# Kernel optimization log

Hardware: AMD Instinct MI355X
Metric: run time of the kernel (lower is better)

## Reference

```python
import jax, jax.numpy as jnp
import numpy as np

H = 64
N_NODES = 12000
N_EDGES = 50000


def setup_inputs() -> dict:
    key = jax.random.key(0)
    ks = jax.random.split(key, 16)
    s = 1.0 / np.sqrt(H)
    inp = {
        "node": jax.random.normal(ks[0], (N_NODES, H), jnp.float32),
        "edge": jax.random.normal(ks[1], (N_EDGES, H), jnp.float32),
        "hidden_feats": jax.random.normal(ks[2], (N_NODES, H), jnp.float32),
        "src": jax.random.randint(ks[3], (N_EDGES,), 0, N_NODES, jnp.int32),
        "dst": jax.random.randint(ks[4], (N_EDGES,), 0, N_NODES, jnp.int32),
        # edge_network: Linear(H, 2H) -> ReLU -> Linear(2H, H*H)
        "W1": jax.random.uniform(ks[5], (2 * H, H), jnp.float32, -s, s),
        "b1": jax.random.uniform(ks[6], (2 * H,), jnp.float32, -s, s),
        "W2": jax.random.uniform(ks[7], (H * H, 2 * H), jnp.float32, -1 / np.sqrt(2 * H), 1 / np.sqrt(2 * H)),
        "b2": jax.random.uniform(ks[8], (H * H,), jnp.float32, -1 / np.sqrt(2 * H), 1 / np.sqrt(2 * H)),
        # GRUCell params (torch layout: [3H, H], gate order r,z,n)
        "W_ih": jax.random.uniform(ks[9], (3 * H, H), jnp.float32, -s, s),
        "W_hh": jax.random.uniform(ks[10], (3 * H, H), jnp.float32, -s, s),
        "b_ih": jax.random.uniform(ks[11], (3 * H,), jnp.float32, -s, s),
        "b_hh": jax.random.uniform(ks[12], (3 * H,), jnp.float32, -s, s),
        # LayerNorm params
        "gamma": jnp.ones((H,), jnp.float32),
        "beta": jnp.zeros((H,), jnp.float32),
    }
    return inp


def _gru_cell(x, h, W_ih, W_hh, b_ih, b_hh):
    gi = x @ W_ih.T + b_ih  # [N, 3H]
    gh = h @ W_hh.T + b_hh  # [N, 3H]
    r = jax.nn.sigmoid(gi[:, :H] + gh[:, :H])
    z = jax.nn.sigmoid(gi[:, H:2 * H] + gh[:, H:2 * H])
    n = jnp.tanh(gi[:, 2 * H:] + r * gh[:, 2 * H:])
    return (1.0 - z) * n + z * h


def reference(node, edge, hidden_feats, src, dst, W1, b1, W2, b2,
              W_ih, W_hh, b_ih, b_hh, gamma, beta):
    n_nodes = node.shape[0]
    # edge network -> per-edge [H,H] weight matrices
    eh = jax.nn.relu(edge @ W1.T + b1)                      # [E, 2H]
    Wedge = (eh @ W2.T + b2).reshape(-1, H, H)              # [E, H, H]
    # gather src feats, per-edge matmul (row-vector @ matrix), scatter-sum to dst
    msg = jnp.einsum('eh,ehk->ek', node[src], Wedge)        # [E, H]
    agg = jax.ops.segment_sum(msg, dst, num_segments=n_nodes)  # [N, H]
    new_node_feats = jax.nn.relu(agg)
    out = _gru_cell(new_node_feats, hidden_feats, W_ih, W_hh, b_ih, b_hh)
    # LayerNorm (eps=1e-5)
    mu = jnp.mean(out, axis=-1, keepdims=True)
    var = jnp.var(out, axis=-1, keepdims=True)
    out = (out - mu) * jax.lax.rsqrt(var + 1e-5) * gamma + beta
    return out
```

## Files before the change

### kernel.cpp

```cpp
#include <hip/hip_runtime.h>

#define H 64
#define NEDGE 50000
#define NNODE 12000
#define EPAD 50176

typedef _Float16 f16;
typedef _Float16 h8 __attribute__((ext_vector_type(8)));
typedef float f4 __attribute__((ext_vector_type(4)));
typedef float fv16 __attribute__((ext_vector_type(16)));

#define O_EDGEH 0ull
#define O_W2G   6422528ull
#define O_B2G   7471104ull
#define O_W1G   7479296ull
#define O_WG    7495680ull
#define O_AGG   7561216ull

__device__ __forceinline__ fv16 zero16() {
  fv16 z;
#pragma unroll
  for (int i = 0; i < 16; ++i) z[i] = 0.f;
  return z;
}

__global__ __launch_bounds__(256) void k_prep(const float* __restrict__ edge, const float* __restrict__ W1,
                                              const float* __restrict__ W2, const float* __restrict__ b2,
                                              const float* __restrict__ Wih, const float* __restrict__ Whh,
                                              f16* __restrict__ edgeh, f16* __restrict__ w1g, f16* __restrict__ w2g,
                                              f16* __restrict__ b2g, f16* __restrict__ wg, float* __restrict__ agg) {
  int bid = blockIdx.x;
  int t = threadIdx.x;
  if (bid < 750) {
    int id = bid * 256 + t;
    *(f4*)(agg + (long)id * 4) = (f4){0.f, 0.f, 0.f, 0.f};
    return;
  }
  if (bid < 2318) {
    long id8 = (long)(bid - 750) * 256 + t;
    long e = id8 >> 3;
    int c = (int)(id8 & 7) * 8;
    h8 o = {};
    if (e < NEDGE) {
      const float* p = edge + e * 64 + c;
      f4 v0 = *(const f4*)p, v1 = *(const f4*)(p + 4);
#pragma unroll
      for (int j = 0; j < 4; ++j) { o[j] = (f16)v0[j]; o[4 + j] = (f16)v1[j]; }
    }
    *(h8*)(edgeh + e * 64 + c) = o;
    return;
  }
  if (bid < 4366) {
    int id = (bid - 2318) * 256 + t;
    int i = id & 7, l = (id >> 3) & 63, nh = (id >> 9) & 1, s = (id >> 10) & 7, h = id >> 13;
    int n = nh * 32 + (l & 31), j = s * 16 + ((l >> 5) << 3) + i;
    w2g[id] = (f16)W2[(h * 64 + n) * 128 + j];
    return;
  }
  if (bid < 4382) {
    int id = (bid - 4366) * 256 + t;
    int i = id & 7, l = (id >> 3) & 63, nh = (id >> 9) & 1, s = id >> 10;
    int n = nh * 32 + (l & 31), k = s * 16 + ((l >> 5) << 3) + i;
    b2g[id] = (f16)b2[k * 64 + n];
    return;
  }
  if (bid < 4414) {
    int id = (bid - 4382) * 256 + t;
    int i = id & 7, l = (id >> 3) & 63, nt = (id >> 9) & 3, s = id >> 11;
    int n = nt * 32 + (l & 31), k = s * 16 + ((l >> 5) << 3) + i;
    w1g[id] = (f16)W1[n * 64 + k];
    return;
  }
  {
    int id = (bid - 4414) * 256 + t;
    int ii = id & 7, l = (id >> 3) & 63, tt = (id >> 9) & 15, s = id >> 13;
    int k = s * 32 + ((l >> 4) << 3) + ii, n = tt * 16 + (l & 15);
    float v;
    if (n < 128) v = (k < 64) ? Wih[n * 64 + k] : Whh[n * 64 + (k - 64)];
    else if (n < 192) v = (k < 64) ? Wih[n * 64 + k] : 0.f;
    else v = (k < 64) ? 0.f : Whh[(n - 64) * 64 + (k - 64)];
    wg[id] = (f16)v;
  }
}

__global__ __launch_bounds__(256, 3) void k_msg(const float* __restrict__ node,
                                                const int* __restrict__ src, const int* __restrict__ dst,
                                                const f16* __restrict__ edgeh, const f16* __restrict__ w1g,
                                                const f16* __restrict__ w2g, const float* __restrict__ b1,
                                                float* __restrict__ agg) {
  __shared__ __align__(16) char lds[26368];
  f16* eh_s = (f16*)lds;
  f16* vT = (f16*)(lds + 16384);
  int* sdst = (int*)(lds + 25600);
  float* b1s = (float*)(lds + 25856);

  int t = threadIdx.x;
  int bid = blockIdx.x;
  int e_base = (bid >> 1) * 64;
  int hs = bid & 1;

  if (t < 64) {
    int eg = e_base + t;
    sdst[t] = (eg < NEDGE) ? dst[eg] : 0;
  } else if (t < 192) {
    b1s[t - 64] = b1[t - 64];
  }
  {
    int m = t >> 2, q = t & 3;
    int eg = e_base + m;
    int si = (eg < NEDGE) ? src[eg] : 0;
    const f4* nr = (const f4*)(node + (long)si * 64 + q * 16);
    f4 v0 = nr[0], v1 = nr[1], v2 = nr[2], v3 = nr[3];
    h8 p0, p1;
#pragma unroll
    for (int j = 0; j < 4; ++j) {
      p0[j] = (f16)v0[j]; p0[4 + j] = (f16)v1[j];
      p1[j] = (f16)v2[j]; p1[4 + j] = (f16)v3[j];
    }
    *(h8*)(vT + m * 72 + q * 16) = p0;
    *(h8*)(vT + m * 72 + q * 16 + 8) = p1;
  }
  __syncthreads();

  int wave = t >> 6, lane = t & 63;
  int l31 = lane & 31, lh = lane >> 5;
  int kh = wave & 1, wn = wave >> 1;

  {
    h8 afr[2][4];
#pragma unroll
    for (int mt = 0; mt < 2; ++mt)
#pragma unroll
      for (int s = 0; s < 4; ++s)
        afr[mt][s] = *(const h8*)(edgeh + (long)(e_base + mt * 32 + l31) * 64 + s * 16 + lh * 8);
    h8 bfr[4];
#pragma unroll
    for (int s = 0; s < 4; ++s)
      bfr[s] = *(const h8*)(w1g + ((s * 4 + wave) * 64 + lane) * 8);
    fv16 acc_eh[2];
    acc_eh[0] = zero16(); acc_eh[1] = zero16();
#pragma unroll
    for (int s = 0; s < 4; ++s)
#pragma unroll
      for (int mt = 0; mt < 2; ++mt)
        acc_eh[mt] = __builtin_amdgcn_mfma_f32_32x32x16_f16(afr[mt][s], bfr[s], acc_eh[mt], 0, 0, 0);
#pragma unroll
    for (int mt = 0; mt < 2; ++mt)
#pragma unroll
      for (int r = 0; r < 16; ++r) {
        int row = (r & 3) + 8 * (r >> 2) + 4 * lh;
        int e = mt * 32 + row;
        int n = wave * 32 + l31;
        float val = fmaxf(acc_eh[mt][r] + b1s[n], 0.f);
        int o = n >> 3;
        eh_s[e * 128 + ((o ^ (e & 15)) << 3) + (n & 7)] = (f16)val;
      }
  }
  __syncthreads();

  h8 ehreg[2][4];
#pragma unroll
  for (int mt = 0; mt < 2; ++mt) {
    int e = mt * 32 + l31;
#pragma unroll
    for (int s = 0; s < 4; ++s) {
      int o = ((kh * 4 + s) * 2 + lh) ^ (e & 15);
      ehreg[mt][s] = *(const h8*)(eh_s + e * 128 + o * 8);
    }
  }
  __syncthreads();

  fv16 acc[2];
  acc[0] = zero16(); acc[1] = zero16();
  const f16* vrow = vT + l31 * 72;

  const f16* bb = w2g + kh * 4096 + wn * 512 + (long)lane * 8;
  int hfirst = hs << 5;
  int hlast = hfirst + 31;

  h8 bA[4], bB[4];
#pragma unroll
  for (int s = 0; s < 4; ++s) bA[s] = *(const h8*)(bb + (long)hfirst * 8192 + s * 1024);

  auto step = [&](h8 (&bc)[4], h8 (&bn)[4], int h, f16 v0, f16 v1) {
    if (h < hlast) {
      const f16* bp = bb + (long)(h + 1) * 8192;
#pragma unroll
      for (int s = 0; s < 4; ++s) bn[s] = *(const h8*)(bp + s * 1024);
    }
#pragma unroll
    for (int s = 0; s < 4; ++s) {
      h8 bf = bc[s];
      h8 a0 = ehreg[0][s] * v0;
      acc[0] = __builtin_amdgcn_mfma_f32_32x32x16_f16(a0, bf, acc[0], 0, 0, 0);
      h8 a1 = ehreg[1][s] * v1;
      acc[1] = __builtin_amdgcn_mfma_f32_32x32x16_f16(a1, bf, acc[1], 0, 0, 0);
    }
  };

#pragma unroll 1
  for (int hb = hs * 4; hb < hs * 4 + 4; ++hb) {
    h8 vh0 = *(const h8*)(vrow + hb * 8);
    h8 vh1 = *(const h8*)(vrow + 32 * 72 + hb * 8);
#pragma unroll
    for (int hh = 0; hh < 8; ++hh) {
      int h = hb * 8 + hh;
      if (hh & 1) step(bB, bA, h, vh0[hh], vh1[hh]);
      else step(bA, bB, h, vh0[hh], vh1[hh]);
    }
  }

  if (hs) {
    const f16* bt = w2g + (long)64 * 8192 + kh * 2048 + wn * 512 + (long)lane * 8;
#pragma unroll
    for (int sw = 0; sw < 2; ++sw) {
      h8 bf = *(const h8*)(bt + sw * 1024);
#pragma unroll
      for (int mt = 0; mt < 2; ++mt) {
        h8 a = *(const h8*)(vrow + mt * 32 * 72 + ((kh * 2 + sw) * 2 + lh) * 8);
        acc[mt] = __builtin_amdgcn_mfma_f32_32x32x16_f16(a, bf, acc[mt], 0, 0, 0);
      }
    }
  }

  {
    float* red = (float*)lds;
    float* mybase = red + wave * 1024;
    auto wr = [&](const fv16& a) {
#pragma unroll
      for (int r = 0; r < 4; ++r) {
        f4 q = {a[4 * r], a[4 * r + 1], a[4 * r + 2], a[4 * r + 3]};
        *(f4*)(mybase + r * 256 + lane * 4) = q;
      }
    };
    if (!kh) wr(acc[1]); else wr(acc[0]);
    __syncthreads();
    const float* pb = red + (wave ^ 1) * 1024;
    auto rd = [&](fv16& a) {
#pragma unroll
      for (int r = 0; r < 4; ++r) {
        f4 q = *(const f4*)(pb + r * 256 + lane * 4);
        a[4 * r] += q[0]; a[4 * r + 1] += q[1]; a[4 * r + 2] += q[2]; a[4 * r + 3] += q[3];
      }
    };
    if (!kh) rd(acc[0]); else rd(acc[1]);
  }

  {
    int n = wn * 32 + l31;
    const fv16& a = kh ? acc[1] : acc[0];
#pragma unroll
    for (int r = 0; r < 16; ++r) {
      int el = kh * 32 + (r & 3) + 8 * (r >> 2) + 4 * lh;
      if (e_base + el < NEDGE) atomicAdd(&agg[(long)sdst[el] * 64 + n], a[r]);
    }
  }
}

__global__ __launch_bounds__(256) void k_node(const float* __restrict__ agg, const float* __restrict__ hid,
                                              const f16* __restrict__ wg,
                                              const float* __restrict__ bih, const float* __restrict__ bhh,
                                              const float* __restrict__ gamma, const float* __restrict__ beta,
                                              float* __restrict__ out) {
  __shared__ __align__(16) f16 xh_s[128 * 136];
  __shared__ float bsum[128], bin_s[64], bhn_s[64], gam_s[64], bet_s[64];
  int t = threadIdx.x;
  int n0 = blockIdx.x * 128;

  if (t < 128) bsum[t] = bih[t] + bhh[t];
  else if (t < 192) bin_s[t - 128] = bih[t];
  else bhn_s[t - 192] = bhh[t - 64];
  if (t < 64) gam_s[t] = gamma[t];
  else if (t < 128) bet_s[t - 64] = beta[t - 64];

  {
    int m = t >> 1, half = t & 1;
    int mg = n0 + m;
    bool vld = mg < NNODE;
    const float* sp = half ? (hid + (long)mg * 64) : (agg + (long)mg * 64);
#pragma unroll
    for (int jj = 0; jj < 8; ++jj) {
      f4 v0 = {0, 0, 0, 0}, v1 = {0, 0, 0, 0};
      if (vld) { v0 = *(const f4*)(sp + jj * 8); v1 = *(const f4*)(sp + jj * 8 + 4); }
      h8 pk;
#pragma unroll
      for (int m2 = 0; m2 < 4; ++m2) {
        pk[m2] = (f16)(half ? v0[m2] : fmaxf(v0[m2], 0.f));
        pk[4 + m2] = (f16)(half ? v1[m2] : fmaxf(v1[m2], 0.f));
      }
      *(h8*)(xh_s + m * 136 + half * 64 + jj * 8) = pk;
    }
  }
  __syncthreads();

  int wave = t >> 6, lane = t & 63;
  int l15 = lane & 15, lq = lane >> 4;

  f4 acc[2][16];
#pragma unroll
  for (int g = 0; g < 2; ++g)
#pragma unroll
    for (int tt = 0; tt < 16; ++tt) acc[g][tt] = (f4){0.f, 0.f, 0.f, 0.f};

#pragma unroll
  for (int s = 0; s < 4; ++s) {
    h8 a0 = *(const h8*)(xh_s + (wave * 32 + l15) * 136 + s * 32 + lq * 8);
    h8 a1 = *(const h8*)(xh_s + (wave * 32 + 16 + l15) * 136 + s * 32 + lq * 8);
#pragma unroll
    for (int tt = 0; tt < 16; ++tt) {
      h8 b = *(const h8*)(wg + ((s * 16 + tt) * 64 + lane) * 8);
      acc[0][tt] = __builtin_amdgcn_mfma_f32_16x16x32_f16(a0, b, acc[0][tt], 0, 0, 0);
      acc[1][tt] = __builtin_amdgcn_mfma_f32_16x16x32_f16(a1, b, acc[1][tt], 0, 0, 0);
    }
  }

#pragma unroll
  for (int g = 0; g < 2; ++g)
#pragma unroll
    for (int r = 0; r < 4; ++r) {
      int mg = n0 + wave * 32 + g * 16 + lq * 4 + r;
      bool vld = mg < NNODE;
      float o[4], ssum = 0.f, s2 = 0.f;
#pragma unroll
      for (int t0 = 0; t0 < 4; ++t0) {
        int f = t0 * 16 + l15;
        float rpre = acc[g][t0][r] + bsum[f];
        float zpre = acc[g][4 + t0][r] + bsum[64 + f];
        float ginv = acc[g][8 + t0][r] + bin_s[f];
        float ghnv = acc[g][12 + t0][r] + bhn_s[f];
        float rr = 1.f / (1.f + __expf(-rpre));
        float zz = 1.f / (1.f + __expf(-zpre));
        float hv = vld ? hid[(long)mg * 64 + f] : 0.f;
        float nn = tanhf(ginv + rr * ghnv);
        float oo = (1.f - zz) * nn + zz * hv;
        o[t0] = oo; ssum += oo; s2 += oo * oo;
      }
#pragma unroll
      for (int d = 1; d < 16; d <<= 1) {
        ssum += __shfl_xor(ssum, d);
        s2 += __shfl_xor(s2, d);
      }
      float mu = ssum * (1.f / 64.f);
      float var = s2 * (1.f / 64.f) - mu * mu;
      float rstd = rsqrtf(var + 1e-5f);
      if (vld)
#pragma unroll
        for (int t0 = 0; t0 < 4; ++t0) {
          int f = t0 * 16 + l15;
          out[(long)mg * 64 + f] = (o[t0] - mu) * rstd * gam_s[f] + bet_s[f];
        }
    }
}

extern "C" void kernel_launch(void* const* d_in, const int* in_sizes, int n_in,
                              void* d_out, int out_size, void* d_ws, size_t ws_size,
                              hipStream_t stream) {
  const float* node = (const float*)d_in[0];
  const float* edge = (const float*)d_in[1];
  const float* hid = (const float*)d_in[2];
  const int* src = (const int*)d_in[3];
  const int* dst = (const int*)d_in[4];
  const float* W1 = (const float*)d_in[5];
  const float* b1 = (const float*)d_in[6];
  const float* W2 = (const float*)d_in[7];
  const float* b2 = (const float*)d_in[8];
  const float* Wih = (const float*)d_in[9];
  const float* Whh = (const float*)d_in[10];
  const float* bih = (const float*)d_in[11];
  const float* bhh = (const float*)d_in[12];
  const float* gamma = (const float*)d_in[13];
  const float* beta = (const float*)d_in[14];

  char* ws = (char*)d_ws;
  f16* edgeh = (f16*)(ws + O_EDGEH);
  f16* w2g = (f16*)(ws + O_W2G);
  f16* b2g = (f16*)(ws + O_B2G);
  f16* w1g = (f16*)(ws + O_W1G);
  f16* wg = (f16*)(ws + O_WG);
  float* agg = (float*)(ws + O_AGG);

  k_prep<<<4542, 256, 0, stream>>>(edge, W1, W2, b2, Wih, Whh, edgeh, w1g, w2g, b2g, wg, agg);
  k_msg<<<1564, 256, 0, stream>>>(node, src, dst, edgeh, w1g, w2g, b1, agg);
  k_node<<<94, 256, 0, stream>>>(agg, hid, wg, bih, bhh, gamma, beta, (float*)d_out);
}
```

Measured before the change: 188.8 us.

## Process all H slices per block, split K across four waves with full N tiles

Each k_msg block now handles all 64 h-slices of the W2-derived per-edge weight for its 64 edges instead of splitting h across two blocks. The grid is halved and the per-block edge-network and gather prologue is no longer duplicated. Each wave now owns a quarter of the K dimension and computes both N halves for both M tiles, which means four accumulators per wave and a multi-stage LDS reduction across waves. The aim is to cut redundant prologue work and reuse each A fragment across two MFMAs. The cost is more registers, fewer blocks in flight and extra barriers in the reduction.

```diff
diff --git a/kernel.cpp b/kernel.cpp
--- a/kernel.cpp
+++ b/kernel.cpp
@@ -95,9 +95,7 @@
   float* b1s = (float*)(lds + 25856);
 
   int t = threadIdx.x;
-  int bid = blockIdx.x;
-  int e_base = (bid >> 1) * 64;
-  int hs = bid & 1;
+  int e_base = blockIdx.x * 64;
 
   if (t < 64) {
     int eg = e_base + t;
@@ -124,7 +122,8 @@
 
   int wave = t >> 6, lane = t & 63;
   int l31 = lane & 31, lh = lane >> 5;
-  int kh = wave & 1, wn = wave >> 1;
+  int kq = wave;
+  int nhk = wave & 1, mtk = wave >> 1;
 
   {
     h8 afr[2][4];
@@ -158,50 +157,49 @@
   }
   __syncthreads();
 
-  h8 ehreg[2][4];
+  h8 ehreg[2][2];
 #pragma unroll
   for (int mt = 0; mt < 2; ++mt) {
     int e = mt * 32 + l31;
 #pragma unroll
-    for (int s = 0; s < 4; ++s) {
-      int o = ((kh * 4 + s) * 2 + lh) ^ (e & 15);
+    for (int s = 0; s < 2; ++s) {
+      int o = ((kq * 2 + s) * 2 + lh) ^ (e & 15);
       ehreg[mt][s] = *(const h8*)(eh_s + e * 128 + o * 8);
     }
   }
   __syncthreads();
 
-  fv16 acc[2];
-  acc[0] = zero16(); acc[1] = zero16();
+  fv16 acc[2][2];
+  acc[0][0] = zero16(); acc[0][1] = zero16(); acc[1][0] = zero16(); acc[1][1] = zero16();
   const f16* vrow = vT + l31 * 72;
 
-  const f16* bb = w2g + kh * 4096 + wn * 512 + (long)lane * 8;
-  int hfirst = hs << 5;
-  int hlast = hfirst + 31;
+  const char* bb = (const char*)w2g + kq * 4096 + (long)lane * 16;
 
   h8 bA[4], bB[4];
 #pragma unroll
-  for (int s = 0; s < 4; ++s) bA[s] = *(const h8*)(bb + (long)hfirst * 8192 + s * 1024);
+  for (int q = 0; q < 4; ++q) bA[q] = *(const h8*)(bb + q * 1024);
 
   auto step = [&](h8 (&bc)[4], h8 (&bn)[4], int h, f16 v0, f16 v1) {
-    if (h < hlast) {
-      const f16* bp = bb + (long)(h + 1) * 8192;
-#pragma unroll
-      for (int s = 0; s < 4; ++s) bn[s] = *(const h8*)(bp + s * 1024);
-    }
-#pragma unroll
-    for (int s = 0; s < 4; ++s) {
-      h8 bf = bc[s];
+    if (h < 63) {
+      const char* bp = bb + (long)(h + 1) * 16384;
+#pragma unroll
+      for (int q = 0; q < 4; ++q) bn[q] = *(const h8*)(bp + q * 1024);
+    }
+#pragma unroll
+    for (int s = 0; s < 2; ++s) {
       h8 a0 = ehreg[0][s] * v0;
-      acc[0] = __builtin_amdgcn_mfma_f32_32x32x16_f16(a0, bf, acc[0], 0, 0, 0);
       h8 a1 = ehreg[1][s] * v1;
-      acc[1] = __builtin_amdgcn_mfma_f32_32x32x16_f16(a1, bf, acc[1], 0, 0, 0);
+      acc[0][0] = __builtin_amdgcn_mfma_f32_32x32x16_f16(a0, bc[s * 2 + 0], acc[0][0], 0, 0, 0);
+      acc[0][1] = __builtin_amdgcn_mfma_f32_32x32x16_f16(a0, bc[s * 2 + 1], acc[0][1], 0, 0, 0);
+      acc[1][0] = __builtin_amdgcn_mfma_f32_32x32x16_f16(a1, bc[s * 2 + 0], acc[1][0], 0, 0, 0);
+      acc[1][1] = __builtin_amdgcn_mfma_f32_32x32x16_f16(a1, bc[s * 2 + 1], acc[1][1], 0, 0, 0);
     }
   };
 
 #pragma unroll 1
-  for (int hb = hs * 4; hb < hs * 4 + 4; ++hb) {
+  for (int hb = 0; hb < 8; ++hb) {
     h8 vh0 = *(const h8*)(vrow + hb * 8);
-    h8 vh1 = *(const h8*)(vrow + 32 * 72 + hb * 8);
+    h8 vh1 = *(const h8*)(vrow + 2304 + hb * 8);
 #pragma unroll
     for (int hh = 0; hh < 8; ++hh) {
       int h = hb * 8 + hh;
@@ -210,49 +208,61 @@
     }
   }
 
-  if (hs) {
-    const f16* bt = w2g + (long)64 * 8192 + kh * 2048 + wn * 512 + (long)lane * 8;
-#pragma unroll
-    for (int sw = 0; sw < 2; ++sw) {
-      h8 bf = *(const h8*)(bt + sw * 1024);
-#pragma unroll
-      for (int mt = 0; mt < 2; ++mt) {
-        h8 a = *(const h8*)(vrow + mt * 32 * 72 + ((kh * 2 + sw) * 2 + lh) * 8);
-        acc[mt] = __builtin_amdgcn_mfma_f32_32x32x16_f16(a, bf, acc[mt], 0, 0, 0);
-      }
+  {
+    const char* btb = (const char*)w2g + (long)64 * 16384 + kq * 2048 + (long)lane * 16;
+    h8 bt0 = *(const h8*)(btb);
+    h8 bt1 = *(const h8*)(btb + 1024);
+#pragma unroll
+    for (int mt = 0; mt < 2; ++mt) {
+      h8 a = *(const h8*)(vrow + mt * 2304 + (kq * 2 + lh) * 8);
+      acc[mt][0] = __builtin_amdgcn_mfma_f32_32x32x16_f16(a, bt0, acc[mt][0], 0, 0, 0);
+      acc[mt][1] = __builtin_amdgcn_mfma_f32_32x32x16_f16(a, bt1, acc[mt][1], 0, 0, 0);
     }
   }
 
   {
     float* red = (float*)lds;
-    float* mybase = red + wave * 1024;
-    auto wr = [&](const fv16& a) {
+    float* myp = red + wave * 1024;
+    auto wrtile = [&](const fv16& a) {
 #pragma unroll
       for (int r = 0; r < 4; ++r) {
         f4 q = {a[4 * r], a[4 * r + 1], a[4 * r + 2], a[4 * r + 3]};
-        *(f4*)(mybase + r * 256 + lane * 4) = q;
+        *(f4*)(myp + r * 256 + lane * 4) = q;
       }
     };
-    if (!kh) wr(acc[1]); else wr(acc[0]);
-    __syncthreads();
-    const float* pb = red + (wave ^ 1) * 1024;
-    auto rd = [&](fv16& a) {
+    auto addtile = [&](fv16& a, const float* p) {
 #pragma unroll
       for (int r = 0; r < 4; ++r) {
-        f4 q = *(const f4*)(pb + r * 256 + lane * 4);
+        f4 q = *(const f4*)(p + r * 256 + lane * 4);
         a[4 * r] += q[0]; a[4 * r + 1] += q[1]; a[4 * r + 2] += q[2]; a[4 * r + 3] += q[3];
       }
     };
-    if (!kh) rd(acc[0]); else rd(acc[1]);
-  }
-
-  {
-    int n = wn * 32 + l31;
-    const fv16& a = kh ? acc[1] : acc[0];
+    const float* p1 = red + (wave ^ 1) * 1024;
+    const float* p3 = red + (wave ^ 2) * 1024;
+    if (!nhk) wrtile(acc[0][1]); else wrtile(acc[0][0]);
+    __syncthreads();
+    if (!nhk) addtile(acc[0][0], p1); else addtile(acc[0][1], p1);
+    __syncthreads();
+    if (!nhk) wrtile(acc[1][1]); else wrtile(acc[1][0]);
+    __syncthreads();
+    if (!nhk) addtile(acc[1][0], p1); else addtile(acc[1][1], p1);
+    __syncthreads();
+    if (!mtk) { if (!nhk) wrtile(acc[1][0]); else wrtile(acc[1][1]); }
+    else      { if (!nhk) wrtile(acc[0][0]); else wrtile(acc[0][1]); }
+    __syncthreads();
+    if (!mtk) { if (!nhk) addtile(acc[0][0], p3); else addtile(acc[0][1], p3); }
+    else      { if (!nhk) addtile(acc[1][0], p3); else addtile(acc[1][1], p3); }
+  }
+
+  {
+    fv16 av;
+    if (!mtk) { if (!nhk) av = acc[0][0]; else av = acc[0][1]; }
+    else      { if (!nhk) av = acc[1][0]; else av = acc[1][1]; }
+    int n = nhk * 32 + l31;
 #pragma unroll
     for (int r = 0; r < 16; ++r) {
-      int el = kh * 32 + (r & 3) + 8 * (r >> 2) + 4 * lh;
-      if (e_base + el < NEDGE) atomicAdd(&agg[(long)sdst[el] * 64 + n], a[r]);
+      int el = mtk * 32 + (r & 3) + 8 * (r >> 2) + 4 * lh;
+      if (e_base + el < NEDGE) atomicAdd(&agg[(long)sdst[el] * 64 + n], av[r]);
     }
   }
 }
@@ -380,6 +390,6 @@
   float* agg = (float*)(ws + O_AGG);
 
   k_prep<<<4542, 256, 0, stream>>>(edge, W1, W2, b2, Wih, Whh, edgeh, w1g, w2g, b2g, wg, agg);
-  k_msg<<<1564, 256, 0, stream>>>(node, src, dst, edgeh, w1g, w2g, b1, agg);
+  k_msg<<<782, 256, 0, stream>>>(node, src, dst, edgeh, w1g, w2g, b1, agg);
   k_node<<<94, 256, 0, stream>>>(agg, hid, wg, bih, bhh, gamma, beta, (float*)d_out);
 }
```

New measurement: 243.3 us. 1.29x slower.
